# Performance work log

Hardware: AMD Instinct MI355X
Metric: run time of the kernel (lower is better)

Reference implementation:

```python
import jax, jax.numpy as jnp
import numpy as np

B, D, H = 8192, 1024, 1024


def _linear_init(key, shape, fan_in):
    bound = 1.0 / np.sqrt(fan_in)
    return jax.random.uniform(key, shape, jnp.float32, -bound, bound)


def setup_inputs() -> dict:
    key = jax.random.key(0)
    ks = jax.random.split(key, 20)
    inp = {
        "x": jax.random.normal(ks[0], (B, D), jnp.float32),
        "h_prev": jax.random.normal(ks[1], (B, H), jnp.float32),
        "c_prev": jax.random.normal(ks[2], (B, H), jnp.float32),
        "C_prev": jax.random.normal(ks[3], (B, H), jnp.float32),
        "n_prev": jax.random.uniform(ks[4], (B, H), jnp.float32),
        "m_prev": jax.random.normal(ks[5], (B, H), jnp.float32),
    }
    # input projections Wz/Wi/Wf/Wo: Linear(D -> H) with bias
    for i, g in enumerate("ziofo"[:4]):
        pass
    names = ["z", "i", "f", "o"]
    for j, g in enumerate(names):
        inp[f"W{g}"] = _linear_init(ks[6 + j], (H, D), D)
        inp[f"b{g}"] = _linear_init(ks[10 + j], (H,), D)
        inp[f"R{g}"] = _linear_init(ks[14 + j], (H, H), H)  # no bias
    return inp


def reference(x, h_prev, c_prev, C_prev, n_prev, m_prev,
              Wz, bz, Wi, bi, Wf, bf, Wo, bo,
              Rz, Ri, Rf, Ro):
    # Batch the 4 input projections and 4 recurrent projections into 2 GEMMs.
    Wcat = jnp.concatenate([Wi, Wf, Wo, Wz], axis=0)        # [4H, D]
    bcat = jnp.concatenate([bi, bf, bo, bz], axis=0)        # [4H]
    Rcat = jnp.concatenate([Ri, Rf, Ro, Rz], axis=0)        # [4H, H]
    pre = x @ Wcat.T + bcat + h_prev @ Rcat.T               # [B, 4H]
    pi, pf, po, pz = jnp.split(pre, 4, axis=1)

    i = jnp.exp(pi)
    f = jax.nn.sigmoid(pf)
    o = jax.nn.sigmoid(po)
    z = jnp.tanh(pz)

    c = f * c_prev + i * z
    n = f * n_prev + i
    m = jnp.maximum(jnp.log(f) + m_prev, pi)  # log(exp(pi)) == pi
    h = o * (c / n)
    return (h, c, C_prev, n, m)
```

## Files before the change

kernel.cpp:

```cpp
#include <hip/hip_runtime.h>


#define B_SZ 8192
#define D_SZ 1024
#define H_SZ 1024
#define K_SZ 2048
#define N4H  4096

typedef __attribute__((ext_vector_type(4))) float f32x4;
typedef _Float16 f16;
typedef __attribute__((ext_vector_type(8))) f16 f16x8;
typedef unsigned short u16;
typedef __attribute__((ext_vector_type(4))) unsigned short u16x4;

static __device__ __forceinline__ u16 f2h(float f) {
    f16 h = (f16)f;
    return __builtin_bit_cast(unsigned short, h);
}

static __device__ __forceinline__ void load_lds16(const void* g, void* l) {
    __builtin_amdgcn_global_load_lds(
        (const __attribute__((address_space(1))) void*)g,
        (__attribute__((address_space(3))) void*)l, 16, 0, 0);
}

__global__ void convert_AW(const float* __restrict__ x, const float* __restrict__ h,
                           const float* __restrict__ Wi, const float* __restrict__ Wf,
                           const float* __restrict__ Wo, const float* __restrict__ Wz,
                           const float* __restrict__ Ri, const float* __restrict__ Rf,
                           const float* __restrict__ Ro, const float* __restrict__ Rz,
                           u16* __restrict__ A, u16* __restrict__ Wb) {
    const size_t nvecA = (size_t)B_SZ * K_SZ / 4;
    const size_t nvecW = (size_t)N4H * K_SZ / 4;
    const size_t nvec  = nvecA + nvecW;
    const size_t stride = (size_t)gridDim.x * blockDim.x;
    for (size_t v = (size_t)blockIdx.x * blockDim.x + threadIdx.x; v < nvec; v += stride) {
        const float* src;
        u16* dst;
        if (v < nvecA) {
            size_t e = v * 4;
            size_t row = e >> 11;
            int col = (int)(e & 2047);
            src = (col < D_SZ) ? (x + row * D_SZ + col)
                               : (h + row * H_SZ + (col - D_SZ));
            dst = A + e;
        } else {
            size_t e = (v - nvecA) * 4;
            size_t r = e >> 11;
            int col = (int)(e & 2047);
            int g = (int)(r >> 4) & 3;
            int j = (int)((r >> 6) << 4) | (int)(r & 15);
            const float* Wg = (g == 0) ? Wi : (g == 1) ? Wf : (g == 2) ? Wo : Wz;
            const float* Rg = (g == 0) ? Ri : (g == 1) ? Rf : (g == 2) ? Ro : Rz;
            src = (col < D_SZ) ? (Wg + (size_t)j * D_SZ + col)
                               : (Rg + (size_t)j * H_SZ + (col - D_SZ));
            dst = Wb + e;
        }
        f32x4 val = *(const f32x4*)src;
        u16x4 o;
        o[0] = f2h(val[0]); o[1] = f2h(val[1]); o[2] = f2h(val[2]); o[3] = f2h(val[3]);
        *(u16x4*)dst = o;
    }
}

__global__ __launch_bounds__(256, 2)
void gemm_fused(const u16* __restrict__ A, const u16* __restrict__ W,
                const float* __restrict__ c_prev, const float* __restrict__ C_prev,
                const float* __restrict__ n_prev, const float* __restrict__ m_prev,
                const float* __restrict__ bi, const float* __restrict__ bfv,
                const float* __restrict__ bo, const float* __restrict__ bz,
                float* __restrict__ out) {
    __shared__ u16 lA[128 * 64];
    __shared__ u16 lB[128 * 64];

    const int tid = threadIdx.x;
    const int w  = tid >> 6;
    const int l  = tid & 63;
    const int wm = w >> 1;
    const int wn = w & 1;
    const int m0 = blockIdx.x * 128;
    const int n0 = blockIdx.y * 128;

    const int lrow8 = l >> 3;
    const int lseg  = (l & 7) ^ lrow8;

    const int fr = l & 15;
    const int kq = l >> 4;

    f32x4 acc[4][4] = {};

    for (int kt = 0; kt < K_SZ; kt += 64) {
#pragma unroll
        for (int r = 0; r < 4; ++r) {
            int rowA = r * 32 + w * 8 + lrow8;
            const u16* gA = A + (size_t)(m0 + rowA) * K_SZ + kt + lseg * 8;
            load_lds16(gA, (char*)lA + (r * 32 + w * 8) * 128);
            const u16* gB = W + (size_t)(n0 + rowA) * K_SZ + kt + lseg * 8;
            load_lds16(gB, (char*)lB + (r * 32 + w * 8) * 128);
        }
        __syncthreads();

#pragma unroll
        for (int ks = 0; ks < 2; ++ks) {
            f16x8 af[4], bfr[4];
#pragma unroll
            for (int mi = 0; mi < 4; ++mi) {
                int row = wm * 64 + mi * 16 + fr;
                int seg = (ks * 4 + kq) ^ (row & 7);
                af[mi] = *(const f16x8*)&lA[row * 64 + seg * 8];
            }
#pragma unroll
            for (int ni = 0; ni < 4; ++ni) {
                int row = wn * 64 + ni * 16 + fr;
                int seg = (ks * 4 + kq) ^ (row & 7);
                bfr[ni] = *(const f16x8*)&lB[row * 64 + seg * 8];
            }
            __builtin_amdgcn_s_setprio(1);
#pragma unroll
            for (int mi = 0; mi < 4; ++mi)
#pragma unroll
                for (int ni = 0; ni < 4; ++ni)
                    acc[mi][ni] = __builtin_amdgcn_mfma_f32_16x16x32_f16(
                        af[mi], bfr[ni], acc[mi][ni], 0, 0, 0);
            __builtin_amdgcn_s_setprio(0);
        }
        __syncthreads();
    }

    const size_t BH = (size_t)B_SZ * H_SZ;
    const int j = ((n0 + wn * 64) >> 6) * 16 + fr;
    const float bvi = bi[j], bvf = bfv[j], bvo = bo[j], bvz = bz[j];

#pragma unroll
    for (int mi = 0; mi < 4; ++mi) {
        const int rbase = m0 + wm * 64 + mi * 16 + kq * 4;
        float cp[4], Cp[4], np[4], mp[4];
#pragma unroll
        for (int r2 = 0; r2 < 4; ++r2) {
            const size_t idx = (size_t)(rbase + r2) * H_SZ + j;
            cp[r2] = c_prev[idx];
            Cp[r2] = C_prev[idx];
            np[r2] = n_prev[idx];
            mp[r2] = m_prev[idx];
        }
#pragma unroll
        for (int r2 = 0; r2 < 4; ++r2) {
            const size_t idx = (size_t)(rbase + r2) * H_SZ + j;
            float pi = acc[mi][0][r2] + bvi;
            float pf = acc[mi][1][r2] + bvf;
            float po = acc[mi][2][r2] + bvo;
            float pz = acc[mi][3][r2] + bvz;
            float iv = __expf(pi);
            float fv = 1.0f / (1.0f + __expf(-pf));
            float ov = 1.0f / (1.0f + __expf(-po));
            float e2 = __expf(2.0f * pz);
            float zv = 1.0f - 2.0f / (e2 + 1.0f);
            float cv = fv * cp[r2] + iv * zv;
            float nv = fv * np[r2] + iv;
            float mv = fmaxf(__logf(fv) + mp[r2], pi);
            out[idx]          = ov * (cv / nv);
            out[BH + idx]     = cv;
            out[2 * BH + idx] = Cp[r2];
            out[3 * BH + idx] = nv;
            out[4 * BH + idx] = mv;
        }
    }
}

extern "C" void kernel_launch(void* const* d_in, const int* in_sizes, int n_in,
                              void* d_out, int out_size, void* d_ws, size_t ws_size,
                              hipStream_t stream) {
    const float* x      = (const float*)d_in[0];
    const float* h_prev = (const float*)d_in[1];
    const float* c_prev = (const float*)d_in[2];
    const float* C_prev = (const float*)d_in[3];
    const float* n_prev = (const float*)d_in[4];
    const float* m_prev = (const float*)d_in[5];
    const float* Wz = (const float*)d_in[6];
    const float* bz = (const float*)d_in[7];
    const float* Rz = (const float*)d_in[8];
    const float* Wi = (const float*)d_in[9];
    const float* bi = (const float*)d_in[10];
    const float* Ri = (const float*)d_in[11];
    const float* Wf = (const float*)d_in[12];
    const float* bf = (const float*)d_in[13];
    const float* Rf = (const float*)d_in[14];
    const float* Wo = (const float*)d_in[15];
    const float* bo = (const float*)d_in[16];
    const float* Ro = (const float*)d_in[17];
    float* out = (float*)d_out;

    u16* Abuf = (u16*)d_ws;
    u16* Wbuf = (u16*)((char*)d_ws + (size_t)32 * 1024 * 1024);

    convert_AW<<<2048, 256, 0, stream>>>(x, h_prev, Wi, Wf, Wo, Wz,
                                         Ri, Rf, Ro, Rz, Abuf, Wbuf);

    gemm_fused<<<dim3(B_SZ / 128, N4H / 128), 256, 0, stream>>>(
        Abuf, Wbuf, c_prev, C_prev, n_prev, m_prev, bi, bf, bo, bz, out);
}
```

Before: 218.7 us.

## Rewrite GEMM as 256x256 tile with multi-stage LDS pipeline and XCD-aware block mapping

The fused GEMM moves from a 128x128 tile with 4 waves and single-buffered LDS to a 256x256 tile with 8 waves, triple-buffered A and double-buffered B. Global-to-LDS loads for future k-tiles are interleaved with MFMA quarters using explicit barriers and vmcnt waits. Blocks are remapped so each XCD handles a fixed pair of N-column tiles, which should improve L2 reuse. The aim is to hide load latency and cut global traffic per FLOP. The cost is higher register and LDS pressure at one block per CU, plus a hand-tuned schedule that is fragile.

Measured after the change: 216.2 us. Within noise of the previous version (-1.2%).

```diff
diff --git a/kernel.cpp b/kernel.cpp
--- a/kernel.cpp
+++ b/kernel.cpp
@@ -63,86 +63,138 @@
     }
 }
 
-__global__ __launch_bounds__(256, 2)
+__global__ __launch_bounds__(512, 1)
 void gemm_fused(const u16* __restrict__ A, const u16* __restrict__ W,
                 const float* __restrict__ c_prev, const float* __restrict__ C_prev,
                 const float* __restrict__ n_prev, const float* __restrict__ m_prev,
                 const float* __restrict__ bi, const float* __restrict__ bfv,
                 const float* __restrict__ bo, const float* __restrict__ bz,
                 float* __restrict__ out) {
-    __shared__ u16 lA[128 * 64];
-    __shared__ u16 lB[128 * 64];
+    __shared__ u16 lA[3][256 * 64];
+    __shared__ u16 lB[2][256 * 64];
 
     const int tid = threadIdx.x;
-    const int w  = tid >> 6;
-    const int l  = tid & 63;
-    const int wm = w >> 1;
-    const int wn = w & 1;
-    const int m0 = blockIdx.x * 128;
-    const int n0 = blockIdx.y * 128;
+    const int w   = tid >> 6;
+    const int l   = tid & 63;
+    const int wm  = w >> 2;
+    const int wn  = w & 3;
+
+    const int xcd = blockIdx.x & 7;
+    const int loc = blockIdx.x >> 3;
+    const int bm  = loc & 31;
+    const int bn  = xcd * 2 + (loc >> 5);
+    const int m0  = bm * 256;
+    const int n0r = bn * 256;
 
     const int lrow8 = l >> 3;
-    const int lseg  = (l & 7) ^ lrow8;
+    const int laneOff = lrow8 * K_SZ + ((l & 7) ^ lrow8) * 8;
 
     const int fr = l & 15;
     const int kq = l >> 4;
 
-    f32x4 acc[4][4] = {};
-
-    for (int kt = 0; kt < K_SZ; kt += 64) {
-#pragma unroll
-        for (int r = 0; r < 4; ++r) {
-            int rowA = r * 32 + w * 8 + lrow8;
-            const u16* gA = A + (size_t)(m0 + rowA) * K_SZ + kt + lseg * 8;
-            load_lds16(gA, (char*)lA + (r * 32 + w * 8) * 128);
-            const u16* gB = W + (size_t)(n0 + rowA) * K_SZ + kt + lseg * 8;
-            load_lds16(gB, (char*)lB + (r * 32 + w * 8) * 128);
-        }
-        __syncthreads();
-
-#pragma unroll
-        for (int ks = 0; ks < 2; ++ks) {
-            f16x8 af[4], bfr[4];
-#pragma unroll
-            for (int mi = 0; mi < 4; ++mi) {
-                int row = wm * 64 + mi * 16 + fr;
-                int seg = (ks * 4 + kq) ^ (row & 7);
-                af[mi] = *(const f16x8*)&lA[row * 64 + seg * 8];
+    const u16* Abase = A + (size_t)m0 * K_SZ + laneOff;
+    const u16* Bbase = W + (size_t)n0r * K_SZ + laneOff;
+
+    auto stA = [&](int h, int kt, int s) {
+#pragma unroll
+        for (int r = 0; r < 2; ++r)
+            load_lds16(Abase + (size_t)(h * 128 + r * 64 + w * 8) * K_SZ + kt * 64,
+                       (char*)&lA[s][0] + (h * 128 + r * 64 + w * 8) * 128);
+    };
+    auto stB = [&](int h, int kt, int s) {
+#pragma unroll
+        for (int r = 0; r < 2; ++r)
+            load_lds16(Bbase + (size_t)(h * 128 + r * 64 + w * 8) * K_SZ + kt * 64,
+                       (char*)&lB[s][0] + (h * 128 + r * 64 + w * 8) * 128);
+    };
+
+    f32x4 acc[8][4] = {};
+    f16x8 bf[4][2];
+    f16x8 af[2][2];
+
+    auto rdB = [&](int BS) {
+#pragma unroll
+        for (int ni = 0; ni < 4; ++ni)
+#pragma unroll
+            for (int ks = 0; ks < 2; ++ks) {
+                int row = wn * 64 + ni * 16 + fr;
+                int seg = (ks * 4 + kq) ^ (fr & 7);
+                bf[ni][ks] = *(const f16x8*)&lB[BS][row * 64 + seg * 8];
             }
-#pragma unroll
-            for (int ni = 0; ni < 4; ++ni) {
-                int row = wn * 64 + ni * 16 + fr;
-                int seg = (ks * 4 + kq) ^ (row & 7);
-                bfr[ni] = *(const f16x8*)&lB[row * 64 + seg * 8];
+    };
+    auto rdA = [&](int AS, int q) {
+#pragma unroll
+        for (int mi2 = 0; mi2 < 2; ++mi2)
+#pragma unroll
+            for (int ks = 0; ks < 2; ++ks) {
+                int row = wm * 128 + (q * 2 + mi2) * 16 + fr;
+                int seg = (ks * 4 + kq) ^ (fr & 7);
+                af[mi2][ks] = *(const f16x8*)&lA[AS][row * 64 + seg * 8];
             }
-            __builtin_amdgcn_s_setprio(1);
-#pragma unroll
-            for (int mi = 0; mi < 4; ++mi)
-#pragma unroll
-                for (int ni = 0; ni < 4; ++ni)
-                    acc[mi][ni] = __builtin_amdgcn_mfma_f32_16x16x32_f16(
-                        af[mi], bfr[ni], acc[mi][ni], 0, 0, 0);
-            __builtin_amdgcn_s_setprio(0);
-        }
-        __syncthreads();
+    };
+    auto mfma_q = [&](int q) {
+        __builtin_amdgcn_s_setprio(1);
+#pragma unroll
+        for (int mi2 = 0; mi2 < 2; ++mi2)
+#pragma unroll
+            for (int ni = 0; ni < 4; ++ni)
+#pragma unroll
+                for (int ks = 0; ks < 2; ++ks)
+                    acc[q * 2 + mi2][ni] = __builtin_amdgcn_mfma_f32_16x16x32_f16(
+                        af[mi2][ks], bf[ni][ks], acc[q * 2 + mi2][ni], 0, 0, 0);
+        __builtin_amdgcn_s_setprio(0);
+    };
+
+    auto tile4 = [&](int AS, int BS, int AST, int KT2, int vmmode) {
+        rdA(AS, 0); rdB(BS);
+        if (KT2 >= 0) stA(0, KT2, AST);
+        __builtin_amdgcn_s_barrier();
+        mfma_q(0);
+        __builtin_amdgcn_s_barrier();
+        rdA(AS, 1);
+        if (KT2 >= 0) stA(1, KT2, AST);
+        __builtin_amdgcn_s_barrier();
+        mfma_q(1);
+        __builtin_amdgcn_s_barrier();
+        rdA(AS, 2);
+        if (KT2 >= 0) stB(0, KT2, BS);
+        __builtin_amdgcn_s_barrier();
+        mfma_q(2);
+        __builtin_amdgcn_s_barrier();
+        rdA(AS, 3);
+        if (KT2 >= 0) stB(1, KT2, BS);
+        __builtin_amdgcn_s_barrier();
+        mfma_q(3);
+        if (vmmode == 8)      asm volatile("s_waitcnt vmcnt(8)" ::: "memory");
+        else if (vmmode == 0) asm volatile("s_waitcnt vmcnt(0)" ::: "memory");
+        __builtin_amdgcn_s_barrier();
+    };
+
+    stA(0, 0, 0); stA(1, 0, 0); stB(0, 0, 0); stB(1, 0, 0);
+    stA(0, 1, 1); stA(1, 1, 1); stB(0, 1, 1); stB(1, 1, 1);
+    asm volatile("s_waitcnt vmcnt(8)" ::: "memory");
+    __builtin_amdgcn_s_barrier();
+
+#pragma unroll 1
+    for (int g = 0; g < 5; ++g) {
+        const int T0 = 6 * g;
+        tile4(0, 0, 2, T0 + 2, 8);
+        tile4(1, 1, 0, T0 + 3, 8);
+        tile4(2, 0, 1, T0 + 4, 8);
+        tile4(0, 1, 2, T0 + 5, 8);
+        tile4(1, 0, 0, T0 + 6, 8);
+        tile4(2, 1, 1, T0 + 7, 8);
     }
+    tile4(0, 0, 0, -1, 0);
+    tile4(1, 1, 0, -1, -1);
 
     const size_t BH = (size_t)B_SZ * H_SZ;
-    const int j = ((n0 + wn * 64) >> 6) * 16 + fr;
+    const int j = ((n0r + wn * 64) >> 6) * 16 + fr;
     const float bvi = bi[j], bvf = bfv[j], bvo = bo[j], bvz = bz[j];
 
 #pragma unroll
-    for (int mi = 0; mi < 4; ++mi) {
-        const int rbase = m0 + wm * 64 + mi * 16 + kq * 4;
-        float cp[4], Cp[4], np[4], mp[4];
-#pragma unroll
-        for (int r2 = 0; r2 < 4; ++r2) {
-            const size_t idx = (size_t)(rbase + r2) * H_SZ + j;
-            cp[r2] = c_prev[idx];
-            Cp[r2] = C_prev[idx];
-            np[r2] = n_prev[idx];
-            mp[r2] = m_prev[idx];
-        }
+    for (int mi = 0; mi < 8; ++mi) {
+        const int rbase = m0 + wm * 128 + mi * 16 + kq * 4;
 #pragma unroll
         for (int r2 = 0; r2 < 4; ++r2) {
             const size_t idx = (size_t)(rbase + r2) * H_SZ + j;
@@ -155,12 +207,12 @@
             float ov = 1.0f / (1.0f + __expf(-po));
             float e2 = __expf(2.0f * pz);
             float zv = 1.0f - 2.0f / (e2 + 1.0f);
-            float cv = fv * cp[r2] + iv * zv;
-            float nv = fv * np[r2] + iv;
-            float mv = fmaxf(__logf(fv) + mp[r2], pi);
+            float cv = fv * c_prev[idx] + iv * zv;
+            float nv = fv * n_prev[idx] + iv;
+            float mv = fmaxf(__logf(fv) + m_prev[idx], pi);
             out[idx]          = ov * (cv / nv);
             out[BH + idx]     = cv;
-            out[2 * BH + idx] = Cp[r2];
+            out[2 * BH + idx] = C_prev[idx];
             out[3 * BH + idx] = nv;
             out[4 * BH + idx] = mv;
         }
@@ -196,6 +248,6 @@
     convert_AW<<<2048, 256, 0, stream>>>(x, h_prev, Wi, Wf, Wo, Wz,
                                          Ri, Rf, Ro, Rz, Abuf, Wbuf);
 
-    gemm_fused<<<dim3(B_SZ / 128, N4H / 128), 256, 0, stream>>>(
+    gemm_fused<<<dim3(512), 512, 0, stream>>>(
         Abuf, Wbuf, c_prev, C_prev, n_prev, m_prev, bi, bf, bo, bz, out);
 }
```
